# Performance work log

Hardware: AMD Instinct MI355X
Metric: run time of the kernel (lower is better)

The kernel has to match this reference:

```python
import jax, jax.numpy as jnp
import numpy as np

B, LK, D, H = 16, 4096, 1024, 16
DK = D // H
EPS = 1e-5
NEG = -1.0e9


def _layernorm(x, g, b):
    m = jnp.mean(x, axis=-1, keepdims=True)
    v = jnp.mean((x - m) ** 2, axis=-1, keepdims=True)
    return (x - m) * jax.lax.rsqrt(v + EPS) * g + b


def setup_inputs() -> dict:
    key0 = jax.random.key(0)
    ks = jax.random.split(key0, 12)

    def lin(k, fan_in, fan_out):
        # torch nn.Linear default-ish scale; stored as [in, out] so y = x @ W + b
        return jax.random.normal(k, (fan_in, fan_out), jnp.float32) / np.float32(np.sqrt(fan_in))

    return {
        "query": jax.random.normal(ks[0], (B, 1, D), jnp.float32),
        "key": jax.random.normal(ks[1], (B, LK, D), jnp.float32),
        "mask": jax.random.randint(ks[2], (B, 1, LK), 0, 2, jnp.int32),
        "Wq": lin(ks[3], D, D), "bq": jnp.zeros((D,), jnp.float32),
        "Wk": lin(ks[4], D, D), "bk": jnp.zeros((D,), jnp.float32),
        "Wv": lin(ks[5], D, D), "bv": jnp.zeros((D,), jnp.float32),
        "Wo": lin(ks[6], D, D), "bo": jnp.zeros((D,), jnp.float32),
        "raw_thr": jnp.full((H, 1, 1), 0.1, jnp.float32),
        "Wvp": lin(ks[7], 2 * D, D),  # v_proj, no bias
        "W1": lin(ks[8], D, 2 * D), "b1": jnp.zeros((2 * D,), jnp.float32),
        "W2": lin(ks[9], 2 * D, D), "b2": jnp.zeros((D,), jnp.float32),
        "g1": jnp.ones((D,), jnp.float32), "be1": jnp.zeros((D,), jnp.float32),
        "g2": jnp.ones((D,), jnp.float32), "be2": jnp.zeros((D,), jnp.float32),
    }


def reference(query, key, mask, Wq, bq, Wk, bk, Wv, bv, Wo, bo, raw_thr,
              Wvp, W1, b1, W2, b2, g1, be1, g2, be2):
    b = query.shape[0]
    lk = key.shape[1]
    # v = cat(key, query.repeat(1, Lk, 1)) @ Wvp   (query has seq_len 1)
    v_in = jnp.concatenate([key, jnp.broadcast_to(query, (b, lk, D))], axis=2)
    v = v_in @ Wvp  # [B, Lk, D]

    Q = (query @ Wq + bq).reshape(b, 1, H, DK).transpose(0, 2, 1, 3)   # [B,H,1,DK]
    K = (key @ Wk + bk).reshape(b, lk, H, DK).transpose(0, 2, 1, 3)    # [B,H,Lk,DK]
    V = (v @ Wv + bv).reshape(b, lk, H, DK).transpose(0, 2, 1, 3)      # [B,H,Lk,DK]

    scores = jnp.einsum("bhqd,bhkd->bhqk", Q, K) / jnp.sqrt(jnp.float32(DK))
    # padding mask: [B,1,Lk] -> [B,1,1,Lk]
    scores = jnp.where(mask[:, None] == 0, NEG, scores)
    # learned per-head threshold: softplus(raw_thr) -> [1,H,1,1]
    thr = jax.nn.softplus(raw_thr)[None]
    scores = jnp.where(scores <= thr, NEG, scores)
    attn = jax.nn.softmax(scores, axis=-1)

    x = jnp.einsum("bhqk,bhkd->bhqd", attn, V)            # [B,H,1,DK]
    x = x.transpose(0, 2, 1, 3).reshape(b, 1, H * DK)      # [B,1,D]
    attn_out = x @ Wo + bo

    x = _layernorm(query + attn_out, g1, be1)
    ff = jax.nn.relu(x @ W1 + b1) @ W2 + b2
    x = _layernorm(x + ff, g2, be2)
    return x
```

## Files before the change

kernel.cpp:

```cpp
#include <hip/hip_runtime.h>
#include <hip/hip_bf16.h>

#define NB 16
#define NHD 16
#define ND 1024
#define NLK 4096
#define NFF 2048

typedef float f32x4 __attribute__((ext_vector_type(4)));
typedef __bf16 bf16x8 __attribute__((ext_vector_type(8)));

__device__ inline unsigned enc_f(float f) {
  unsigned u = __float_as_uint(f);
  return (u & 0x80000000u) ? ~u : (u | 0x80000000u);
}
__device__ inline float dec_f(unsigned u) {
  return __uint_as_float((u & 0x80000000u) ? (u & 0x7fffffffu) : ~u);
}

__global__ void k_fill(float* out, int n, float v) {
  int i = blockIdx.x * 256 + threadIdx.x;
  if (i < n) out[i] = v;
}

__global__ __launch_bounds__(256) void k00(const float* __restrict__ query,
                                           const float* __restrict__ raw_thr,
                                           float* __restrict__ q_t,
                                           float* __restrict__ thr) {
  int t = blockIdx.x * 256 + threadIdx.x;
  for (int idx = t; idx < NB * ND; idx += gridDim.x * 256) {
    int b = idx >> 10, i = idx & 1023;
    q_t[i * NB + b] = query[idx];
  }
  if (t < NHD) thr[t] = log1pf(expf(raw_thr[t]));
}

__global__ __launch_bounds__(256) void k0a(const float* __restrict__ Wq,
                                           const float* __restrict__ bq,
                                           const float* __restrict__ Wvp,
                                           const float* __restrict__ q_t,
                                           float* __restrict__ Qrow,
                                           float* __restrict__ cvec) {
  int which = blockIdx.z;
  int j = blockIdx.x * 256 + threadIdx.x;
  int i0 = blockIdx.y * 64;
  float acc[16];
#pragma unroll
  for (int q = 0; q < 16; ++q) acc[q] = 0.f;
  for (int ii = 0; ii < 64; ++ii) {
    int i = i0 + ii;
    float wv = which ? Wvp[(size_t)(ND + i) * ND + j] : Wq[(size_t)i * ND + j];
    float qv[16];
    const float4* qp = (const float4*)(q_t + i * NB);
    *(float4*)&qv[0] = qp[0];
    *(float4*)&qv[4] = qp[1];
    *(float4*)&qv[8] = qp[2];
    *(float4*)&qv[12] = qp[3];
#pragma unroll
    for (int q = 0; q < 16; ++q) acc[q] += wv * qv[q];
  }
  float* out = which ? cvec : Qrow;
  float bias = (!which && blockIdx.y == 0) ? bq[j] : 0.f;
#pragma unroll
  for (int q = 0; q < 16; ++q) atomicAdd(&out[q * ND + j], acc[q] + bias);
}

__global__ __launch_bounds__(256) void k0b(const float* __restrict__ Wk,
                                           const float* __restrict__ Qrow,
                                           __hip_bfloat16* __restrict__ t_bf) {
  int h = blockIdx.x;
  int d0 = blockIdx.y * 128;
  int t = threadIdx.x;
  __shared__ float qs[16 * 64];
  __shared__ float wks[128 * 66];
  {
    int lin = t * 4;
    int b = lin >> 6, dk = lin & 63;
    *(float4*)&qs[b * 64 + dk] = *(const float4*)(Qrow + b * ND + h * 64 + dk);
  }
#pragma unroll
  for (int e = 0; e < 8; ++e) {
    int lin = e * 1024 + t * 4;
    int d = lin >> 6, dk = lin & 63;
    *(float4*)&wks[d * 66 + dk] = *(const float4*)(Wk + (size_t)(d0 + d) * ND + h * 64 + dk);
  }
  __syncthreads();
  int d = t >> 1, bh = (t & 1) * 8;
  float acc[8];
#pragma unroll
  for (int q = 0; q < 8; ++q) acc[q] = 0.f;
  for (int dk = 0; dk < 64; ++dk) {
    float wv = wks[d * 66 + dk];
#pragma unroll
    for (int q = 0; q < 8; ++q) acc[q] += wv * qs[(bh + q) * 64 + dk];
  }
#pragma unroll
  for (int q = 0; q < 8; ++q)
    t_bf[(size_t)((bh + q) * 16 + h) * ND + d0 + d] = (__hip_bfloat16)acc[q];
}

__global__ __launch_bounds__(256) void k0c(const float* __restrict__ bk,
                                           const float* __restrict__ Qrow,
                                           float* __restrict__ s0) {
  int t = threadIdx.x;
  int b = t >> 4, h = t & 15;
  const float* qb = Qrow + b * ND + h * 64;
  const float* bkh = bk + h * 64;
  float acc = 0.f;
  for (int jj = 0; jj < 64; ++jj) acc += bkh[jj] * qb[jj];
  s0[t] = acc;
}

__global__ __launch_bounds__(256) void k_scores(const float* __restrict__ key,
                                                const __hip_bfloat16* __restrict__ t_bf,
                                                const float* __restrict__ s0,
                                                const float* __restrict__ thr,
                                                const int* __restrict__ mask,
                                                float* __restrict__ sc,
                                                unsigned* __restrict__ gmax) {
  int b = blockIdx.y;
  int tid = threadIdx.x;
  int wave = tid >> 6, lane = tid & 63;
  int l15 = lane & 15, g4 = lane >> 4;
  int row = blockIdx.x * 64 + wave * 16 + l15;
  const float* keyb = key + (size_t)b * NLK * ND;
  const __hip_bfloat16* tb = t_bf + (size_t)(b * 16 + l15) * ND;
  f32x4 acc = {0.f, 0.f, 0.f, 0.f};
  for (int ks = 0; ks < 32; ++ks) {
    int dbase = ks * 32 + g4 * 8;
    const float* ap = keyb + (size_t)row * ND + dbase;
    float a[8];
    *(float4*)&a[0] = *(const float4*)ap;
    *(float4*)&a[4] = *(const float4*)(ap + 4);
    bf16x8 af;
#pragma unroll
    for (int j = 0; j < 8; ++j) af[j] = (__bf16)a[j];
    bf16x8 bfr = *(const bf16x8*)(tb + dbase);
    acc = __builtin_amdgcn_mfma_f32_16x16x32_bf16(af, bfr, acc, 0, 0, 0);
  }
  float s0v = s0[b * NHD + l15];
  float thv = thr[l15];
  float lmax = -3.4e38f;
  int rowbase = blockIdx.x * 64 + wave * 16 + g4 * 4;
#pragma unroll
  for (int r = 0; r < 4; ++r) {
    int k = rowbase + r;
    float s = (acc[r] + s0v) * 0.125f;
    int mv = mask[b * NLK + k];
    float o = (mv != 0 && s > thv) ? s : -1.0e9f;
    sc[((size_t)b * NLK + k) * NHD + l15] = o;
    lmax = fmaxf(lmax, o);
  }
  lmax = fmaxf(lmax, __shfl_xor(lmax, 16, 64));
  lmax = fmaxf(lmax, __shfl_xor(lmax, 32, 64));
  if (lane < 16) atomicMax(&gmax[b * NHD + lane], enc_f(lmax));
}

__global__ __launch_bounds__(256) void k_rexp(float* __restrict__ sc,
                                              const unsigned* __restrict__ gmax,
                                              float* __restrict__ lsum) {
  int b = blockIdx.y, kc = blockIdx.x;
  int t = threadIdx.x;
  float* scb = sc + ((size_t)b * NLK + kc * 256) * NHD;
  float m = dec_f(gmax[b * NHD + (t & 15)]);
  float s = 0.f;
#pragma unroll
  for (int i = 0; i < 16; ++i) {
    float v = scb[i * 256 + t];
    float e = expf(v - m);
    scb[i * 256 + t] = e;
    s += e;
  }
  __shared__ float red[16][17];
  red[t >> 4][t & 15] = s;
  __syncthreads();
  for (int st = 8; st > 0; st >>= 1) {
    if ((t >> 4) < st) red[t >> 4][t & 15] += red[(t >> 4) + st][t & 15];
    __syncthreads();
  }
  if (t < 16) atomicAdd(&lsum[b * NHD + t], red[0][t]);
}

__global__ __launch_bounds__(256) void k_u(const float* __restrict__ key,
                                           const float* __restrict__ w,
                                           const float* __restrict__ lsum,
                                           float* __restrict__ u) {
  int b = blockIdx.z, kc = blockIdx.y;
  int d = (blockIdx.x * 256 + threadIdx.x) * 2;
  const float* keyb = key + (size_t)b * NLK * ND;
  const float* wb = w + (size_t)b * NLK * NHD;
  float acc0[16], acc1[16];
#pragma unroll
  for (int q = 0; q < 16; ++q) { acc0[q] = 0.f; acc1[q] = 0.f; }
  int k0 = kc * 256;
  for (int kk = 0; kk < 256; ++kk) {
    int k = k0 + kk;
    float2 kv = *(const float2*)(keyb + (size_t)k * ND + d);
    float wv[16];
    const float4* wp = (const float4*)(wb + (size_t)k * NHD);
    *(float4*)&wv[0] = wp[0];
    *(float4*)&wv[4] = wp[1];
    *(float4*)&wv[8] = wp[2];
    *(float4*)&wv[12] = wp[3];
#pragma unroll
    for (int q = 0; q < 16; ++q) {
      acc0[q] += wv[q] * kv.x;
      acc1[q] += wv[q] * kv.y;
    }
  }
#pragma unroll
  for (int q = 0; q < 16; ++q) {
    float rl = 1.f / lsum[b * NHD + q];
    atomicAdd(&u[(size_t)(b * 16 + q) * ND + d], acc0[q] * rl);
    atomicAdd(&u[(size_t)(b * 16 + q) * ND + d + 1], acc1[q] * rl);
  }
}

__global__ __launch_bounds__(256) void k_z(const float* __restrict__ u,
                                           const float* __restrict__ Wvp,
                                           float* __restrict__ z) {
  __shared__ float ut[128 * 20];
  int t = threadIdx.x;
  int n = blockIdx.x * 256 + t;
  int m0 = blockIdx.y * 16;
  int k0 = blockIdx.z * 128;
#pragma unroll
  for (int e = 0; e < 8; ++e) {
    int lin = e * 256 + t;
    int m = lin >> 7, kk = lin & 127;
    ut[kk * 20 + m] = u[(size_t)(m0 + m) * ND + k0 + kk];
  }
  __syncthreads();
  float acc[16];
#pragma unroll
  for (int q = 0; q < 16; ++q) acc[q] = 0.f;
  for (int kk = 0; kk < 128; ++kk) {
    float wv = Wvp[(size_t)(k0 + kk) * ND + n];
    float uv[16];
    const float4* up = (const float4*)&ut[kk * 20];
    *(float4*)&uv[0] = up[0];
    *(float4*)&uv[4] = up[1];
    *(float4*)&uv[8] = up[2];
    *(float4*)&uv[12] = up[3];
#pragma unroll
    for (int q = 0; q < 16; ++q) acc[q] += wv * uv[q];
  }
#pragma unroll
  for (int q = 0; q < 16; ++q) atomicAdd(&z[(size_t)(m0 + q) * ND + n], acc[q]);
}

__global__ __launch_bounds__(256) void k_attnx(const float* __restrict__ z,
                                               const float* __restrict__ cvec,
                                               const float* __restrict__ Wv,
                                               const float* __restrict__ bv,
                                               float* __restrict__ attn_x) {
  __shared__ float vb[16 * 132];
  int h = blockIdx.x;
  int d0 = blockIdx.y * 128;
  int t = threadIdx.x;
#pragma unroll
  for (int e = 0; e < 8; ++e) {
    int lin = e * 256 + t;
    int bb = lin >> 7, dd = lin & 127;
    vb[bb * 132 + dd] =
        z[(size_t)(bb * 16 + h) * ND + d0 + dd] + cvec[(size_t)bb * ND + d0 + dd];
  }
  __syncthreads();
  int joff = t & 63, bg = t >> 6;
  int j = h * 64 + joff;
  float acc[4] = {0.f, 0.f, 0.f, 0.f};
  for (int dd = 0; dd < 128; ++dd) {
    float wv = Wv[(size_t)(d0 + dd) * ND + j];
#pragma unroll
    for (int q = 0; q < 4; ++q) acc[q] += wv * vb[(bg * 4 + q) * 132 + dd];
  }
#pragma unroll
  for (int q = 0; q < 4; ++q) {
    float val = acc[q];
    if (blockIdx.y == 0) val += bv[j];
    atomicAdd(&attn_x[(size_t)(bg * 4 + q) * ND + j], val);
  }
}

__global__ __launch_bounds__(256) void k_r1(const float* __restrict__ attn_x,
                                            const float* __restrict__ Wo,
                                            const float* __restrict__ bo,
                                            const float* __restrict__ query,
                                            float* __restrict__ r1) {
  __shared__ float ax[16 * 68];
  int j0 = blockIdx.x * 128;
  int d0 = blockIdx.y * 64;
  int t = threadIdx.x;
  {
    int lin = t * 4;
    int bb = lin >> 6, dd = lin & 63;
    *(float4*)&ax[bb * 68 + dd] = *(const float4*)(attn_x + (size_t)bb * ND + d0 + dd);
  }
  __syncthreads();
  int joff = t & 127, bg = t >> 7;
  int j = j0 + joff;
  float acc[8];
#pragma unroll
  for (int q = 0; q < 8; ++q) acc[q] = 0.f;
  for (int dd = 0; dd < 64; ++dd) {
    float wv = Wo[(size_t)(d0 + dd) * ND + j];
#pragma unroll
    for (int q = 0; q < 8; ++q) acc[q] += wv * ax[(bg * 8 + q) * 68 + dd];
  }
#pragma unroll
  for (int q = 0; q < 8; ++q) {
    int bb = bg * 8 + q;
    float val = acc[q];
    if (blockIdx.y == 0) val += bo[j] + query[(size_t)bb * ND + j];
    atomicAdd(&r1[(size_t)bb * ND + j], val);
  }
}

__global__ __launch_bounds__(256) void k_ln1(const float* __restrict__ r1,
                                             const float* __restrict__ g1,
                                             const float* __restrict__ be1,
                                             float* __restrict__ x1) {
  int b = blockIdx.x, t = threadIdx.x;
  __shared__ float rs[256], rs2[256];
  float v[4];
  float s = 0.f, s2 = 0.f;
#pragma unroll
  for (int e = 0; e < 4; ++e) {
    v[e] = r1[(size_t)b * ND + t + 256 * e];
    s += v[e];
    s2 += v[e] * v[e];
  }
  rs[t] = s;
  rs2[t] = s2;
  __syncthreads();
  for (int st = 128; st > 0; st >>= 1) {
    if (t < st) {
      rs[t] += rs[t + st];
      rs2[t] += rs2[t + st];
    }
    __syncthreads();
  }
  float mean = rs[0] * (1.f / ND);
  float var = rs2[0] * (1.f / ND) - mean * mean;
  float inv = rsqrtf(var + 1e-5f);
#pragma unroll
  for (int e = 0; e < 4; ++e) {
    int j = t + 256 * e;
    x1[(size_t)b * ND + j] = (v[e] - mean) * inv * g1[j] + be1[j];
  }
}

__global__ __launch_bounds__(256) void k_ff1(const float* __restrict__ x1,
                                             const float* __restrict__ W1,
                                             float* __restrict__ h1) {
  __shared__ float xs[16 * 68];
  int n = blockIdx.x * 256 + threadIdx.x;
  int d0 = blockIdx.y * 64;
  int t = threadIdx.x;
  {
    int lin = t * 4;
    int bb = lin >> 6, dd = lin & 63;
    *(float4*)&xs[bb * 68 + dd] = *(const float4*)(x1 + (size_t)bb * ND + d0 + dd);
  }
  __syncthreads();
  float acc[16];
#pragma unroll
  for (int q = 0; q < 16; ++q) acc[q] = 0.f;
  for (int dd = 0; dd < 64; ++dd) {
    float wv = W1[(size_t)(d0 + dd) * NFF + n];
#pragma unroll
    for (int q = 0; q < 16; ++q) acc[q] += wv * xs[q * 68 + dd];
  }
#pragma unroll
  for (int q = 0; q < 16; ++q) atomicAdd(&h1[(size_t)q * NFF + n], acc[q]);
}

__global__ __launch_bounds__(256) void k_ff2(const float* __restrict__ h1,
                                             const float* __restrict__ b1,
                                             const float* __restrict__ W2,
                                             float* __restrict__ out2) {
  __shared__ float hs[16 * 132];
  int j0 = blockIdx.x * 128;
  int n0 = blockIdx.y * 128;
  int t = threadIdx.x;
#pragma unroll
  for (int e = 0; e < 8; ++e) {
    int lin = e * 256 + t;
    int bb = lin >> 7, nn = lin & 127;
    float hv = h1[(size_t)bb * NFF + n0 + nn] + b1[n0 + nn];
    hs[bb * 132 + nn] = fmaxf(hv, 0.f);
  }
  __syncthreads();
  int joff = t & 127, bg = t >> 7;
  int j = j0 + joff;
  float acc[8];
#pragma unroll
  for (int q = 0; q < 8; ++q) acc[q] = 0.f;
  for (int nn = 0; nn < 128; ++nn) {
    float wv = W2[(size_t)(n0 + nn) * ND + j];
#pragma unroll
    for (int q = 0; q < 8; ++q) acc[q] += wv * hs[(bg * 8 + q) * 132 + nn];
  }
#pragma unroll
  for (int q = 0; q < 8; ++q) atomicAdd(&out2[(size_t)(bg * 8 + q) * ND + j], acc[q]);
}

__global__ __launch_bounds__(256) void k_ln2(const float* __restrict__ x1,
                                             const float* __restrict__ out2,
                                             const float* __restrict__ b2,
                                             const float* __restrict__ g2,
                                             const float* __restrict__ be2,
                                             float* __restrict__ outp) {
  int b = blockIdx.x, t = threadIdx.x;
  __shared__ float rs[256], rs2[256];
  float v[4];
  float s = 0.f, s2 = 0.f;
#pragma unroll
  for (int e = 0; e < 4; ++e) {
    int j = t + 256 * e;
    v[e] = x1[(size_t)b * ND + j] + out2[(size_t)b * ND + j] + b2[j];
    s += v[e];
    s2 += v[e] * v[e];
  }
  rs[t] = s;
  rs2[t] = s2;
  __syncthreads();
  for (int st = 128; st > 0; st >>= 1) {
    if (t < st) {
      rs[t] += rs[t + st];
      rs2[t] += rs2[t + st];
    }
    __syncthreads();
  }
  float mean = rs[0] * (1.f / ND);
  float var = rs2[0] * (1.f / ND) - mean * mean;
  float inv = rsqrtf(var + 1e-5f);
#pragma unroll
  for (int e = 0; e < 4; ++e) {
    int j = t + 256 * e;
    outp[(size_t)b * ND + j] = (v[e] - mean) * inv * g2[j] + be2[j];
  }
}

extern "C" void kernel_launch(void* const* d_in, const int* in_sizes, int n_in,
                              void* d_out, int out_size, void* d_ws, size_t ws_size,
                              hipStream_t stream) {
  const float* query = (const float*)d_in[0];
  const float* key = (const float*)d_in[1];
  const int* mask = (const int*)d_in[2];
  const float* Wq = (const float*)d_in[3];
  const float* bq = (const float*)d_in[4];
  const float* Wk = (const float*)d_in[5];
  const float* bk = (const float*)d_in[6];
  const float* Wv = (const float*)d_in[7];
  const float* bv = (const float*)d_in[8];
  const float* Wo = (const float*)d_in[9];
  const float* bo = (const float*)d_in[10];
  const float* raw_thr = (const float*)d_in[11];
  const float* Wvp = (const float*)d_in[12];
  const float* W1 = (const float*)d_in[13];
  const float* b1 = (const float*)d_in[14];
  const float* W2 = (const float*)d_in[15];
  const float* b2 = (const float*)d_in[16];
  const float* g1 = (const float*)d_in[17];
  const float* be1 = (const float*)d_in[18];
  const float* g2 = (const float*)d_in[19];
  const float* be2 = (const float*)d_in[20];

  const size_t OFF_QROW = 0;
  const size_t OFF_C = 65536;
  const size_t OFF_ATTNX = 131072;
  const size_t OFF_R1 = 196608;
  const size_t OFF_H1 = 262144;
  const size_t OFF_OUT2 = 393216;
  const size_t OFF_U = 458752;
  const size_t OFF_Z = 1507328;
  const size_t OFF_GMAX = 2555904;
  const size_t OFF_L = 2556928;
  const size_t ZERO_BYTES = 2557952;
  const size_t OFF_X1 = 2557952;
  const size_t OFF_QT = 2623488;
  const size_t OFF_S0 = 2689024;
  const size_t OFF_THR = 2690048;
  const size_t OFF_TBF = 2691072;
  const size_t OFF_SC = 3215360;
  const size_t TOTAL = 7409664;

  if (ws_size < TOTAL) {
    k_fill<<<dim3((out_size + 255) / 256), dim3(256), 0, stream>>>((float*)d_out, out_size,
                                                                   12345.0f);
    return;
  }

  char* wsb = (char*)d_ws;
  float* Qrow = (float*)(wsb + OFF_QROW);
  float* cvec = (float*)(wsb + OFF_C);
  float* attn_x = (float*)(wsb + OFF_ATTNX);
  float* r1 = (float*)(wsb + OFF_R1);
  float* h1 = (float*)(wsb + OFF_H1);
  float* out2 = (float*)(wsb + OFF_OUT2);
  float* u = (float*)(wsb + OFF_U);
  float* z = (float*)(wsb + OFF_Z);
  unsigned* gmax = (unsigned*)(wsb + OFF_GMAX);
  float* lsum = (float*)(wsb + OFF_L);
  float* x1 = (float*)(wsb + OFF_X1);
  float* q_t = (float*)(wsb + OFF_QT);
  float* s0 = (float*)(wsb + OFF_S0);
  float* thr = (float*)(wsb + OFF_THR);
  __hip_bfloat16* t_bf = (__hip_bfloat16*)(wsb + OFF_TBF);
  float* sc = (float*)(wsb + OFF_SC);

  hipMemsetAsync(d_ws, 0, ZERO_BYTES, stream);

  k00<<<dim3(16), dim3(256), 0, stream>>>(query, raw_thr, q_t, thr);
  k0a<<<dim3(4, 16, 2), dim3(256), 0, stream>>>(Wq, bq, Wvp, q_t, Qrow, cvec);
  k0b<<<dim3(16, 8), dim3(256), 0, stream>>>(Wk, Qrow, t_bf);
  k0c<<<dim3(1), dim3(256), 0, stream>>>(bk, Qrow, s0);
  k_scores<<<dim3(64, 16), dim3(256), 0, stream>>>(key, t_bf, s0, thr, mask, sc, gmax);
  k_rexp<<<dim3(16, 16), dim3(256), 0, stream>>>(sc, gmax, lsum);
  k_u<<<dim3(2, 16, 16), dim3(256), 0, stream>>>(key, sc, lsum, u);
  k_z<<<dim3(4, 16, 8), dim3(256), 0, stream>>>(u, Wvp, z);
  k_attnx<<<dim3(16, 8), dim3(256), 0, stream>>>(z, cvec, Wv, bv, attn_x);
  k_r1<<<dim3(8, 16), dim3(256), 0, stream>>>(attn_x, Wo, bo, query, r1);
  k_ln1<<<dim3(16), dim3(256), 0, stream>>>(r1, g1, be1, x1);
  k_ff1<<<dim3(8, 16), dim3(256), 0, stream>>>(x1, W1, h1);
  k_ff2<<<dim3(8, 16), dim3(256), 0, stream>>>(h1, b1, W2, out2);
  k_ln2<<<dim3(16), dim3(256), 0, stream>>>(x1, out2, b2, g2, be2, (float*)d_out);
}
```

Before: 239.2 us.

## Fuse scores, softmax and key-weighted sum into a flash-style split-K kernel

```diff
diff --git a/kernel.cpp b/kernel.cpp
--- a/kernel.cpp
+++ b/kernel.cpp
@@ -8,42 +8,56 @@
 #define NFF 2048
 
 typedef float f32x4 __attribute__((ext_vector_type(4)));
+typedef __bf16 bf16x4v __attribute__((ext_vector_type(4)));
 typedef __bf16 bf16x8 __attribute__((ext_vector_type(8)));
-
-__device__ inline unsigned enc_f(float f) {
-  unsigned u = __float_as_uint(f);
-  return (u & 0x80000000u) ? ~u : (u | 0x80000000u);
-}
-__device__ inline float dec_f(unsigned u) {
-  return __uint_as_float((u & 0x80000000u) ? (u & 0x7fffffffu) : ~u);
-}
 
 __global__ void k_fill(float* out, int n, float v) {
   int i = blockIdx.x * 256 + threadIdx.x;
   if (i < n) out[i] = v;
 }
 
-__global__ __launch_bounds__(256) void k00(const float* __restrict__ query,
-                                           const float* __restrict__ raw_thr,
-                                           float* __restrict__ q_t,
-                                           float* __restrict__ thr) {
-  int t = blockIdx.x * 256 + threadIdx.x;
-  for (int idx = t; idx < NB * ND; idx += gridDim.x * 256) {
-    int b = idx >> 10, i = idx & 1023;
-    q_t[i * NB + b] = query[idx];
-  }
-  if (t < NHD) thr[t] = log1pf(expf(raw_thr[t]));
+__global__ __launch_bounds__(256) void k0t(const float* __restrict__ Wvp,
+                                           __hip_bfloat16* __restrict__ wvpt) {
+  int n0 = blockIdx.x * 64, k0 = blockIdx.y * 64;
+  int t = threadIdx.x;
+  __shared__ float ts[64][68];
+#pragma unroll
+  for (int i = 0; i < 4; ++i) {
+    int idx = t * 4 + i * 1024;
+    int kk = idx >> 6, nn = idx & 63;
+    float4 v = *(const float4*)(Wvp + (size_t)(k0 + kk) * ND + n0 + nn);
+    ts[kk][nn] = v.x; ts[kk][nn + 1] = v.y; ts[kk][nn + 2] = v.z; ts[kk][nn + 3] = v.w;
+  }
+  __syncthreads();
+#pragma unroll
+  for (int i = 0; i < 4; ++i) {
+    int idx = t * 4 + i * 1024;
+    int nn = idx >> 6, kk = idx & 63;
+    bf16x4v o;
+#pragma unroll
+    for (int j = 0; j < 4; ++j) o[j] = (__bf16)ts[kk + j][nn];
+    *(bf16x4v*)((__bf16*)wvpt + (size_t)(n0 + nn) * ND + k0 + kk) = o;
+  }
 }
 
 __global__ __launch_bounds__(256) void k0a(const float* __restrict__ Wq,
                                            const float* __restrict__ bq,
                                            const float* __restrict__ Wvp,
-                                           const float* __restrict__ q_t,
+                                           const float* __restrict__ query,
                                            float* __restrict__ Qrow,
                                            float* __restrict__ cvec) {
   int which = blockIdx.z;
   int j = blockIdx.x * 256 + threadIdx.x;
   int i0 = blockIdx.y * 64;
+  int t = threadIdx.x;
+  __shared__ float qs[64][20];
+  {
+    int e = t * 4;
+    int b = e >> 6, ii = e & 63;
+    float4 v = *(const float4*)(query + (size_t)b * ND + i0 + ii);
+    qs[ii][b] = v.x; qs[ii + 1][b] = v.y; qs[ii + 2][b] = v.z; qs[ii + 3][b] = v.w;
+  }
+  __syncthreads();
   float acc[16];
 #pragma unroll
   for (int q = 0; q < 16; ++q) acc[q] = 0.f;
@@ -51,7 +65,7 @@
     int i = i0 + ii;
     float wv = which ? Wvp[(size_t)(ND + i) * ND + j] : Wq[(size_t)i * ND + j];
     float qv[16];
-    const float4* qp = (const float4*)(q_t + i * NB);
+    const float4* qp = (const float4*)&qs[ii][0];
     *(float4*)&qv[0] = qp[0];
     *(float4*)&qv[4] = qp[1];
     *(float4*)&qv[8] = qp[2];
@@ -66,8 +80,10 @@
 }
 
 __global__ __launch_bounds__(256) void k0b(const float* __restrict__ Wk,
+                                           const float* __restrict__ bk,
                                            const float* __restrict__ Qrow,
-                                           __hip_bfloat16* __restrict__ t_bf) {
+                                           __hip_bfloat16* __restrict__ t_bf,
+                                           float* __restrict__ s0) {
   int h = blockIdx.x;
   int d0 = blockIdx.y * 128;
   int t = threadIdx.x;
@@ -85,6 +101,12 @@
     *(float4*)&wks[d * 66 + dk] = *(const float4*)(Wk + (size_t)(d0 + d) * ND + h * 64 + dk);
   }
   __syncthreads();
+  if (blockIdx.y == 0 && t < 16) {
+    float a = 0.f;
+    const float* bkh = bk + h * 64;
+    for (int jj = 0; jj < 64; ++jj) a += bkh[jj] * qs[t * 64 + jj];
+    s0[t * 16 + h] = a;
+  }
   int d = t >> 1, bh = (t & 1) * 8;
   float acc[8];
 #pragma unroll
@@ -99,154 +121,170 @@
     t_bf[(size_t)((bh + q) * 16 + h) * ND + d0 + d] = (__hip_bfloat16)acc[q];
 }
 
-__global__ __launch_bounds__(256) void k0c(const float* __restrict__ bk,
-                                           const float* __restrict__ Qrow,
-                                           float* __restrict__ s0) {
-  int t = threadIdx.x;
-  int b = t >> 4, h = t & 15;
-  const float* qb = Qrow + b * ND + h * 64;
-  const float* bkh = bk + h * 64;
-  float acc = 0.f;
-  for (int jj = 0; jj < 64; ++jj) acc += bkh[jj] * qb[jj];
-  s0[t] = acc;
-}
-
-__global__ __launch_bounds__(256) void k_scores(const float* __restrict__ key,
-                                                const __hip_bfloat16* __restrict__ t_bf,
-                                                const float* __restrict__ s0,
-                                                const float* __restrict__ thr,
-                                                const int* __restrict__ mask,
-                                                float* __restrict__ sc,
-                                                unsigned* __restrict__ gmax) {
-  int b = blockIdx.y;
-  int tid = threadIdx.x;
-  int wave = tid >> 6, lane = tid & 63;
-  int l15 = lane & 15, g4 = lane >> 4;
-  int row = blockIdx.x * 64 + wave * 16 + l15;
+__global__ __launch_bounds__(256) void k_flash(const float* __restrict__ key,
+                                               const __hip_bfloat16* __restrict__ t_bf,
+                                               const float* __restrict__ s0,
+                                               const float* __restrict__ raw_thr,
+                                               const int* __restrict__ mask,
+                                               float* __restrict__ pu,
+                                               float* __restrict__ mloc,
+                                               float* __restrict__ lloc) {
+  int ch = blockIdx.x, b = blockIdx.y;
+  int t = threadIdx.x;
+  int wv = t >> 6, lane = t & 63, l15 = lane & 15, g4 = lane >> 4;
+  __shared__ float ps[4][32][17];
+  __shared__ float wls[32][16];
+  __shared__ float red[16][16];
+  __shared__ float mrun[16], lrun[16], fact[16], mnew_s[16], thv_s[16], s0_s[16];
+  f32x4 pu_r[16];
+#pragma unroll
+  for (int h = 0; h < 16; ++h) pu_r[h] = (f32x4){0.f, 0.f, 0.f, 0.f};
+  if (t < 16) {
+    mrun[t] = -1.0e9f;
+    lrun[t] = 0.f;
+    thv_s[t] = log1pf(expf(raw_thr[t]));
+    s0_s[t] = s0[b * 16 + t];
+  }
+  __syncthreads();
   const float* keyb = key + (size_t)b * NLK * ND;
   const __hip_bfloat16* tb = t_bf + (size_t)(b * 16 + l15) * ND;
+  int dsl = wv * 256;
+  int dlane = dsl + lane * 4;
+  int k0c = ch * 128;
+  for (int sp = 0; sp < 4; ++sp) {
+    int ks0 = k0c + sp * 32;
+    f32x4 acc0 = {0.f, 0.f, 0.f, 0.f}, acc1 = {0.f, 0.f, 0.f, 0.f};
+    for (int st = 0; st < 8; ++st) {
+      int d = dsl + st * 32 + g4 * 8;
+      bf16x8 bfr = *(const bf16x8*)(tb + d);
+      const float* a0p = keyb + (size_t)(ks0 + l15) * ND + d;
+      const float* a1p = a0p + (size_t)16 * ND;
+      float a0[8], a1[8];
+      *(float4*)&a0[0] = *(const float4*)a0p;
+      *(float4*)&a0[4] = *(const float4*)(a0p + 4);
+      *(float4*)&a1[0] = *(const float4*)a1p;
+      *(float4*)&a1[4] = *(const float4*)(a1p + 4);
+      bf16x8 af0, af1;
+#pragma unroll
+      for (int j = 0; j < 8; ++j) {
+        af0[j] = (__bf16)a0[j];
+        af1[j] = (__bf16)a1[j];
+      }
+      acc0 = __builtin_amdgcn_mfma_f32_16x16x32_bf16(af0, bfr, acc0, 0, 0, 0);
+      acc1 = __builtin_amdgcn_mfma_f32_16x16x32_bf16(af1, bfr, acc1, 0, 0, 0);
+    }
+#pragma unroll
+    for (int r = 0; r < 4; ++r) {
+      ps[wv][g4 * 4 + r][l15] = acc0[r];
+      ps[wv][16 + g4 * 4 + r][l15] = acc1[r];
+    }
+    __syncthreads();
+    int kk0 = t >> 4, hh = t & 15;
+    float sv0, sv1;
+    {
+      float s = (ps[0][kk0][hh] + ps[1][kk0][hh] + ps[2][kk0][hh] + ps[3][kk0][hh] +
+                 s0_s[hh]) * 0.125f;
+      int mv = mask[b * NLK + ks0 + kk0];
+      sv0 = (mv != 0 && s > thv_s[hh]) ? s : -1.0e9f;
+    }
+    {
+      int k2 = kk0 + 16;
+      float s = (ps[0][k2][hh] + ps[1][k2][hh] + ps[2][k2][hh] + ps[3][k2][hh] +
+                 s0_s[hh]) * 0.125f;
+      int mv = mask[b * NLK + ks0 + k2];
+      sv1 = (mv != 0 && s > thv_s[hh]) ? s : -1.0e9f;
+    }
+    red[kk0][hh] = fmaxf(sv0, sv1);
+    __syncthreads();
+    for (int s2 = 8; s2 > 0; s2 >>= 1) {
+      if (kk0 < s2) red[kk0][hh] = fmaxf(red[kk0][hh], red[kk0 + s2][hh]);
+      __syncthreads();
+    }
+    if (t < 16) {
+      float mn = fmaxf(mrun[t], red[0][t]);
+      mnew_s[t] = mn;
+      fact[t] = expf(mrun[t] - mn);
+      mrun[t] = mn;
+    }
+    __syncthreads();
+    float w0 = expf(sv0 - mnew_s[hh]);
+    float w1 = expf(sv1 - mnew_s[hh]);
+    wls[kk0][hh] = w0;
+    wls[kk0 + 16][hh] = w1;
+    red[kk0][hh] = w0 + w1;
+    __syncthreads();
+    for (int s2 = 8; s2 > 0; s2 >>= 1) {
+      if (kk0 < s2) red[kk0][hh] += red[kk0 + s2][hh];
+      __syncthreads();
+    }
+    if (t < 16) lrun[t] = lrun[t] * fact[t] + red[0][t];
+#pragma unroll
+    for (int h = 0; h < 16; ++h) pu_r[h] *= fact[h];
+    const float* kb2 = keyb + (size_t)ks0 * ND + dlane;
+    for (int k = 0; k < 32; ++k) {
+      f32x4 kv = *(const f32x4*)(kb2 + (size_t)k * ND);
+#pragma unroll
+      for (int h = 0; h < 16; ++h) pu_r[h] += wls[k][h] * kv;
+    }
+    __syncthreads();
+  }
+  size_t pubase = (size_t)((b * 32 + ch) * 16) * ND + dlane;
+#pragma unroll
+  for (int h = 0; h < 16; ++h) *(f32x4*)(pu + pubase + (size_t)h * ND) = pu_r[h];
+  if (t < 16) {
+    mloc[(b * 32 + ch) * 16 + t] = mrun[t];
+    lloc[(b * 32 + ch) * 16 + t] = lrun[t];
+  }
+}
+
+__global__ __launch_bounds__(256) void k_ured(const float* __restrict__ pu,
+                                              const float* __restrict__ mloc,
+                                              const float* __restrict__ lloc,
+                                              __hip_bfloat16* __restrict__ u_bf) {
+  int h = blockIdx.x, b = blockIdx.y;
+  int t = threadIdx.x;
+  __shared__ float sc_s[32];
+  if (t < 32) {
+    float m = mloc[(b * 32 + t) * 16 + h];
+    float l = lloc[(b * 32 + t) * 16 + h];
+    float mg = m;
+    for (int o = 16; o > 0; o >>= 1) mg = fmaxf(mg, __shfl_xor(mg, o, 32));
+    float term = l * expf(m - mg);
+    float ls = term;
+    for (int o = 16; o > 0; o >>= 1) ls += __shfl_xor(ls, o, 32);
+    sc_s[t] = expf(m - mg) / ls;
+  }
+  __syncthreads();
+  int d = t * 4;
+  f32x4 acc = {0.f, 0.f, 0.f, 0.f};
+  for (int c = 0; c < 32; ++c) {
+    f32x4 v = *(const f32x4*)(pu + (size_t)((b * 32 + c) * 16 + h) * ND + d);
+    acc += sc_s[c] * v;
+  }
+  bf16x4v o;
+#pragma unroll
+  for (int j = 0; j < 4; ++j) o[j] = (__bf16)acc[j];
+  *(bf16x4v*)((__bf16*)u_bf + (size_t)(b * 16 + h) * ND + d) = o;
+}
+
+__global__ __launch_bounds__(256) void k_zm(const __hip_bfloat16* __restrict__ u_bf,
+                                            const __hip_bfloat16* __restrict__ wvpt,
+                                            float* __restrict__ z) {
+  int ntg = blockIdx.x, mt = blockIdx.y;
+  int t = threadIdx.x, wv = t >> 6, lane = t & 63, l15 = lane & 15, g4 = lane >> 4;
+  int nt = ntg * 4 + wv;
+  const __hip_bfloat16* ub = u_bf + (size_t)(mt * 16 + l15) * ND;
+  const __hip_bfloat16* wb = wvpt + (size_t)(nt * 16 + l15) * ND;
   f32x4 acc = {0.f, 0.f, 0.f, 0.f};
   for (int ks = 0; ks < 32; ++ks) {
-    int dbase = ks * 32 + g4 * 8;
-    const float* ap = keyb + (size_t)row * ND + dbase;
-    float a[8];
-    *(float4*)&a[0] = *(const float4*)ap;
-    *(float4*)&a[4] = *(const float4*)(ap + 4);
-    bf16x8 af;
-#pragma unroll
-    for (int j = 0; j < 8; ++j) af[j] = (__bf16)a[j];
-    bf16x8 bfr = *(const bf16x8*)(tb + dbase);
-    acc = __builtin_amdgcn_mfma_f32_16x16x32_bf16(af, bfr, acc, 0, 0, 0);
-  }
-  float s0v = s0[b * NHD + l15];
-  float thv = thr[l15];
-  float lmax = -3.4e38f;
-  int rowbase = blockIdx.x * 64 + wave * 16 + g4 * 4;
-#pragma unroll
-  for (int r = 0; r < 4; ++r) {
-    int k = rowbase + r;
-    float s = (acc[r] + s0v) * 0.125f;
-    int mv = mask[b * NLK + k];
-    float o = (mv != 0 && s > thv) ? s : -1.0e9f;
-    sc[((size_t)b * NLK + k) * NHD + l15] = o;
-    lmax = fmaxf(lmax, o);
-  }
-  lmax = fmaxf(lmax, __shfl_xor(lmax, 16, 64));
-  lmax = fmaxf(lmax, __shfl_xor(lmax, 32, 64));
-  if (lane < 16) atomicMax(&gmax[b * NHD + lane], enc_f(lmax));
-}
-
-__global__ __launch_bounds__(256) void k_rexp(float* __restrict__ sc,
-                                              const unsigned* __restrict__ gmax,
-                                              float* __restrict__ lsum) {
-  int b = blockIdx.y, kc = blockIdx.x;
-  int t = threadIdx.x;
-  float* scb = sc + ((size_t)b * NLK + kc * 256) * NHD;
-  float m = dec_f(gmax[b * NHD + (t & 15)]);
-  float s = 0.f;
-#pragma unroll
-  for (int i = 0; i < 16; ++i) {
-    float v = scb[i * 256 + t];
-    float e = expf(v - m);
-    scb[i * 256 + t] = e;
-    s += e;
-  }
-  __shared__ float red[16][17];
-  red[t >> 4][t & 15] = s;
-  __syncthreads();
-  for (int st = 8; st > 0; st >>= 1) {
-    if ((t >> 4) < st) red[t >> 4][t & 15] += red[(t >> 4) + st][t & 15];
-    __syncthreads();
-  }
-  if (t < 16) atomicAdd(&lsum[b * NHD + t], red[0][t]);
-}
-
-__global__ __launch_bounds__(256) void k_u(const float* __restrict__ key,
-                                           const float* __restrict__ w,
-                                           const float* __restrict__ lsum,
-                                           float* __restrict__ u) {
-  int b = blockIdx.z, kc = blockIdx.y;
-  int d = (blockIdx.x * 256 + threadIdx.x) * 2;
-  const float* keyb = key + (size_t)b * NLK * ND;
-  const float* wb = w + (size_t)b * NLK * NHD;
-  float acc0[16], acc1[16];
-#pragma unroll
-  for (int q = 0; q < 16; ++q) { acc0[q] = 0.f; acc1[q] = 0.f; }
-  int k0 = kc * 256;
-  for (int kk = 0; kk < 256; ++kk) {
-    int k = k0 + kk;
-    float2 kv = *(const float2*)(keyb + (size_t)k * ND + d);
-    float wv[16];
-    const float4* wp = (const float4*)(wb + (size_t)k * NHD);
-    *(float4*)&wv[0] = wp[0];
-    *(float4*)&wv[4] = wp[1];
-    *(float4*)&wv[8] = wp[2];
-    *(float4*)&wv[12] = wp[3];
-#pragma unroll
-    for (int q = 0; q < 16; ++q) {
-      acc0[q] += wv[q] * kv.x;
-      acc1[q] += wv[q] * kv.y;
-    }
-  }
-#pragma unroll
-  for (int q = 0; q < 16; ++q) {
-    float rl = 1.f / lsum[b * NHD + q];
-    atomicAdd(&u[(size_t)(b * 16 + q) * ND + d], acc0[q] * rl);
-    atomicAdd(&u[(size_t)(b * 16 + q) * ND + d + 1], acc1[q] * rl);
-  }
-}
-
-__global__ __launch_bounds__(256) void k_z(const float* __restrict__ u,
-                                           const float* __restrict__ Wvp,
-                                           float* __restrict__ z) {
-  __shared__ float ut[128 * 20];
-  int t = threadIdx.x;
-  int n = blockIdx.x * 256 + t;
-  int m0 = blockIdx.y * 16;
-  int k0 = blockIdx.z * 128;
-#pragma unroll
-  for (int e = 0; e < 8; ++e) {
-    int lin = e * 256 + t;
-    int m = lin >> 7, kk = lin & 127;
-    ut[kk * 20 + m] = u[(size_t)(m0 + m) * ND + k0 + kk];
-  }
-  __syncthreads();
-  float acc[16];
-#pragma unroll
-  for (int q = 0; q < 16; ++q) acc[q] = 0.f;
-  for (int kk = 0; kk < 128; ++kk) {
-    float wv = Wvp[(size_t)(k0 + kk) * ND + n];
-    float uv[16];
-    const float4* up = (const float4*)&ut[kk * 20];
-    *(float4*)&uv[0] = up[0];
-    *(float4*)&uv[4] = up[1];
-    *(float4*)&uv[8] = up[2];
-    *(float4*)&uv[12] = up[3];
-#pragma unroll
-    for (int q = 0; q < 16; ++q) acc[q] += wv * uv[q];
-  }
-#pragma unroll
-  for (int q = 0; q < 16; ++q) atomicAdd(&z[(size_t)(m0 + q) * ND + n], acc[q]);
+    int d = ks * 32 + g4 * 8;
+    bf16x8 a = *(const bf16x8*)(ub + d);
+    bf16x8 bb = *(const bf16x8*)(wb + d);
+    acc = __builtin_amdgcn_mfma_f32_16x16x32_bf16(a, bb, acc, 0, 0, 0);
+  }
+#pragma unroll
+  for (int r = 0; r < 4; ++r)
+    z[(size_t)(mt * 16 + g4 * 4 + r) * ND + nt * 16 + l15] = acc[r];
 }
 
 __global__ __launch_bounds__(256) void k_attnx(const float* __restrict__ z,
@@ -316,51 +354,48 @@
   }
 }
 
-__global__ __launch_bounds__(256) void k_ln1(const float* __restrict__ r1,
+__global__ __launch_bounds__(256) void k_ff1(const float* __restrict__ r1,
                                              const float* __restrict__ g1,
                                              const float* __restrict__ be1,
-                                             float* __restrict__ x1) {
-  int b = blockIdx.x, t = threadIdx.x;
-  __shared__ float rs[256], rs2[256];
-  float v[4];
-  float s = 0.f, s2 = 0.f;
-#pragma unroll
-  for (int e = 0; e < 4; ++e) {
-    v[e] = r1[(size_t)b * ND + t + 256 * e];
-    s += v[e];
-    s2 += v[e] * v[e];
-  }
-  rs[t] = s;
-  rs2[t] = s2;
-  __syncthreads();
-  for (int st = 128; st > 0; st >>= 1) {
-    if (t < st) {
-      rs[t] += rs[t + st];
-      rs2[t] += rs2[t + st];
-    }
-    __syncthreads();
-  }
-  float mean = rs[0] * (1.f / ND);
-  float var = rs2[0] * (1.f / ND) - mean * mean;
-  float inv = rsqrtf(var + 1e-5f);
-#pragma unroll
-  for (int e = 0; e < 4; ++e) {
-    int j = t + 256 * e;
-    x1[(size_t)b * ND + j] = (v[e] - mean) * inv * g1[j] + be1[j];
-  }
-}
-
-__global__ __launch_bounds__(256) void k_ff1(const float* __restrict__ x1,
                                              const float* __restrict__ W1,
                                              float* __restrict__ h1) {
-  __shared__ float xs[16 * 68];
   int n = blockIdx.x * 256 + threadIdx.x;
   int d0 = blockIdx.y * 64;
   int t = threadIdx.x;
+  __shared__ float mv_s[16], iv_s[16];
+  __shared__ float xs[16 * 68];
   {
-    int lin = t * 4;
-    int bb = lin >> 6, dd = lin & 63;
-    *(float4*)&xs[bb * 68 + dd] = *(const float4*)(x1 + (size_t)bb * ND + d0 + dd);
+    int row = t >> 4, seg = t & 15;
+    float s = 0.f, s2 = 0.f;
+    const float* rp = r1 + (size_t)row * ND + seg * 64;
+    for (int q = 0; q < 16; ++q) {
+      float4 v = *(const float4*)(rp + q * 4);
+      s += v.x + v.y + v.z + v.w;
+      s2 += v.x * v.x + v.y * v.y + v.z * v.z + v.w * v.w;
+    }
+    for (int o = 1; o < 16; o <<= 1) {
+      s += __shfl_xor(s, o, 16);
+      s2 += __shfl_xor(s2, o, 16);
+    }
+    if (seg == 0) {
+      float mean = s * (1.f / ND);
+      float var = s2 * (1.f / ND) - mean * mean;
+      mv_s[row] = mean;
+      iv_s[row] = rsqrtf(var + 1e-5f);
+    }
+  }
+  __syncthreads();
+  {
+    int e = t * 4;
+    int bb = e >> 6, dd = e & 63;
+    float4 v = *(const float4*)(r1 + (size_t)bb * ND + d0 + dd);
+    float4 g = *(const float4*)(g1 + d0 + dd);
+    float4 be = *(const float4*)(be1 + d0 + dd);
+    float m = mv_s[bb], iv = iv_s[bb];
+    xs[bb * 68 + dd] = (v.x - m) * iv * g.x + be.x;
+    xs[bb * 68 + dd + 1] = (v.y - m) * iv * g.y + be.y;
+    xs[bb * 68 + dd + 2] = (v.z - m) * iv * g.z + be.z;
+    xs[bb * 68 + dd + 3] = (v.w - m) * iv * g.w + be.w;
   }
   __syncthreads();
   float acc[16];
@@ -405,7 +440,9 @@
   for (int q = 0; q < 8; ++q) atomicAdd(&out2[(size_t)(bg * 8 + q) * ND + j], acc[q]);
 }
 
-__global__ __launch_bounds__(256) void k_ln2(const float* __restrict__ x1,
+__global__ __launch_bounds__(256) void k_ln2(const float* __restrict__ r1,
+                                             const float* __restrict__ g1,
+                                             const float* __restrict__ be1,
                                              const float* __restrict__ out2,
                                              const float* __restrict__ b2,
                                              const float* __restrict__ g2,
@@ -413,15 +450,9 @@
                                              float* __restrict__ outp) {
   int b = blockIdx.x, t = threadIdx.x;
   __shared__ float rs[256], rs2[256];
-  float v[4];
-  float s = 0.f, s2 = 0.f;
-#pragma unroll
-  for (int e = 0; e < 4; ++e) {
-    int j = t + 256 * e;
-    v[e] = x1[(size_t)b * ND + j] + out2[(size_t)b * ND + j] + b2[j];
-    s += v[e];
-    s2 += v[e] * v[e];
-  }
+  float4 v = *(const float4*)(r1 + (size_t)b * ND + t * 4);
+  float s = v.x + v.y + v.z + v.w;
+  float s2 = v.x * v.x + v.y * v.y + v.z * v.z + v.w * v.w;
   rs[t] = s;
   rs2[t] = s2;
   __syncthreads();
@@ -435,11 +466,39 @@
   float mean = rs[0] * (1.f / ND);
   float var = rs2[0] * (1.f / ND) - mean * mean;
   float inv = rsqrtf(var + 1e-5f);
-#pragma unroll
-  for (int e = 0; e < 4; ++e) {
-    int j = t + 256 * e;
-    outp[(size_t)b * ND + j] = (v[e] - mean) * inv * g2[j] + be2[j];
-  }
+  float4 g = *(const float4*)(g1 + t * 4);
+  float4 be = *(const float4*)(be1 + t * 4);
+  float4 o2 = *(const float4*)(out2 + (size_t)b * ND + t * 4);
+  float4 bb2 = *(const float4*)(b2 + t * 4);
+  float4 v2;
+  v2.x = (v.x - mean) * inv * g.x + be.x + o2.x + bb2.x;
+  v2.y = (v.y - mean) * inv * g.y + be.y + o2.y + bb2.y;
+  v2.z = (v.z - mean) * inv * g.z + be.z + o2.z + bb2.z;
+  v2.w = (v.w - mean) * inv * g.w + be.w + o2.w + bb2.w;
+  __syncthreads();
+  s = v2.x + v2.y + v2.z + v2.w;
+  s2 = v2.x * v2.x + v2.y * v2.y + v2.z * v2.z + v2.w * v2.w;
+  rs[t] = s;
+  rs2[t] = s2;
+  __syncthreads();
+  for (int st = 128; st > 0; st >>= 1) {
+    if (t < st) {
+      rs[t] += rs[t + st];
+      rs2[t] += rs2[t + st];
+    }
+    __syncthreads();
+  }
+  float mean2 = rs[0] * (1.f / ND);
+  float var2 = rs2[0] * (1.f / ND) - mean2 * mean2;
+  float inv2 = rsqrtf(var2 + 1e-5f);
+  float4 gg = *(const float4*)(g2 + t * 4);
+  float4 bbe = *(const float4*)(be2 + t * 4);
+  float4 o;
+  o.x = (v2.x - mean2) * inv2 * gg.x + bbe.x;
+  o.y = (v2.y - mean2) * inv2 * gg.y + bbe.y;
+  o.z = (v2.z - mean2) * inv2 * gg.z + bbe.z;
+  o.w = (v2.w - mean2) * inv2 * gg.w + bbe.w;
+  *(float4*)(outp + (size_t)b * ND + t * 4) = o;
 }
 
 extern "C" void kernel_launch(void* const* d_in, const int* in_sizes, int n_in,
@@ -473,18 +532,16 @@
   const size_t OFF_R1 = 196608;
   const size_t OFF_H1 = 262144;
   const size_t OFF_OUT2 = 393216;
-  const size_t OFF_U = 458752;
-  const size_t OFF_Z = 1507328;
-  const size_t OFF_GMAX = 2555904;
-  const size_t OFF_L = 2556928;
-  const size_t ZERO_BYTES = 2557952;
-  const size_t OFF_X1 = 2557952;
-  const size_t OFF_QT = 2623488;
-  const size_t OFF_S0 = 2689024;
-  const size_t OFF_THR = 2690048;
-  const size_t OFF_TBF = 2691072;
-  const size_t OFF_SC = 3215360;
-  const size_t TOTAL = 7409664;
+  const size_t ZERO_BYTES = 458752;
+  const size_t OFF_S0 = 458752;
+  const size_t OFF_MLOC = 459776;
+  const size_t OFF_LLOC = 492544;
+  const size_t OFF_TBF = 525312;
+  const size_t OFF_UBF = 1049600;
+  const size_t OFF_WVPT = 1573888;
+  const size_t OFF_Z = 3671040;
+  const size_t OFF_PU = 4719616;
+  const size_t TOTAL = 38274048;
 
   if (ws_size < TOTAL) {
     k_fill<<<dim3((out_size + 255) / 256), dim3(256), 0, stream>>>((float*)d_out, out_size,
@@ -499,31 +556,26 @@
   float* r1 = (float*)(wsb + OFF_R1);
   float* h1 = (float*)(wsb + OFF_H1);
   float* out2 = (float*)(wsb + OFF_OUT2);
-  float* u = (float*)(wsb + OFF_U);
+  float* s0 = (float*)(wsb + OFF_S0);
+  float* mloc = (float*)(wsb + OFF_MLOC);
+  float* lloc = (float*)(wsb + OFF_LLOC);
+  __hip_bfloat16* t_bf = (__hip_bfloat16*)(wsb + OFF_TBF);
+  __hip_bfloat16* u_bf = (__hip_bfloat16*)(wsb + OFF_UBF);
+  __hip_bfloat16* wvpt = (__hip_bfloat16*)(wsb + OFF_WVPT);
   float* z = (float*)(wsb + OFF_Z);
-  unsigned* gmax = (unsigned*)(wsb + OFF_GMAX);
-  float* lsum = (float*)(wsb + OFF_L);
-  float* x1 = (float*)(wsb + OFF_X1);
-  float* q_t = (float*)(wsb + OFF_QT);
-  float* s0 = (float*)(wsb + OFF_S0);
-  float* thr = (float*)(wsb + OFF_THR);
-  __hip_bfloat16* t_bf = (__hip_bfloat16*)(wsb + OFF_TBF);
-  float* sc = (float*)(wsb + OFF_SC);
+  float* pu = (float*)(wsb + OFF_PU);
 
   hipMemsetAsync(d_ws, 0, ZERO_BYTES, stream);
 
-  k00<<<dim3(16), dim3(256), 0, stream>>>(query, raw_thr, q_t, thr);
-  k0a<<<dim3(4, 16, 2), dim3(256), 0, stream>>>(Wq, bq, Wvp, q_t, Qrow, cvec);
-  k0b<<<dim3(16, 8), dim3(256), 0, stream>>>(Wk, Qrow, t_bf);
-  k0c<<<dim3(1), dim3(256), 0, stream>>>(bk, Qrow, s0);
-  k_scores<<<dim3(64, 16), dim3(256), 0, stream>>>(key, t_bf, s0, thr, mask, sc, gmax);
-  k_rexp<<<dim3(16, 16), dim3(256), 0, stream>>>(sc, gmax, lsum);
-  k_u<<<dim3(2, 16, 16), dim3(256), 0, stream>>>(key, sc, lsum, u);
-  k_z<<<dim3(4, 16, 8), dim3(256), 0, stream>>>(u, Wvp, z);
+  k0t<<<dim3(16, 16), dim3(256), 0, stream>>>(Wvp, wvpt);
+  k0a<<<dim3(4, 16, 2), dim3(256), 0, stream>>>(Wq, bq, Wvp, query, Qrow, cvec);
+  k0b<<<dim3(16, 8), dim3(256), 0, stream>>>(Wk, bk, Qrow, t_bf, s0);
+  k_flash<<<dim3(32, 16), dim3(256), 0, stream>>>(key, t_bf, s0, raw_thr, mask, pu, mloc, lloc);
+  k_ured<<<dim3(16, 16), dim3(256), 0, stream>>>(pu, mloc, lloc, u_bf);
+  k_zm<<<dim3(16, 16), dim3(256), 0, stream>>>(u_bf, wvpt, z);
   k_attnx<<<dim3(16, 8), dim3(256), 0, stream>>>(z, cvec, Wv, bv, attn_x);
   k_r1<<<dim3(8, 16), dim3(256), 0, stream>>>(attn_x, Wo, bo, query, r1);
-  k_ln1<<<dim3(16), dim3(256), 0, stream>>>(r1, g1, be1, x1);
-  k_ff1<<<dim3(8, 16), dim3(256), 0, stream>>>(x1, W1, h1);
+  k_ff1<<<dim3(8, 16), dim3(256), 0, stream>>>(r1, g1, be1, W1, h1);
   k_ff2<<<dim3(8, 16), dim3(256), 0, stream>>>(h1, b1, W2, out2);
-  k_ln2<<<dim3(16), dim3(256), 0, stream>>>(x1, out2, b2, g2, be2, (float*)d_out);
-}
+  k_ln2<<<dim3(16), dim3(256), 0, stream>>>(r1, g1, be1, out2, b2, g2, be2, (float*)d_out);
+}
```

New measurement: 205.2 us. 1.17x faster.
